# Kernel tuning notes

Hardware: AMD Instinct MI355X
Metric: run time of the kernel (lower is better)

## Reference

```python
import jax, jax.numpy as jnp
import numpy as np

N_NODES = 100000


def gcn_layer(x, edge_index, W, b):
    """PyG GCNConv: h = D^-1/2 (A+I) D^-1/2 (x W) + b, scatter-sum aggregation."""
    n = x.shape[0]
    h = x @ W  # [N, out]
    loop = jnp.arange(n, dtype=edge_index.dtype)
    src = jnp.concatenate([edge_index[0], loop])  # [E+N]
    dst = jnp.concatenate([edge_index[1], loop])
    deg = jax.ops.segment_sum(jnp.ones_like(dst, dtype=h.dtype), dst, num_segments=n)
    dinv = jnp.where(deg > 0, jax.lax.rsqrt(deg), 0.0)
    norm = dinv[src] * dinv[dst]  # [E+N]
    msg = h[src] * norm[:, None]  # gather + scale (largest intermediate)
    out = jax.ops.segment_sum(msg, dst, num_segments=n)
    return out + b


def setup_inputs() -> dict:
    key = jax.random.key(0)
    k = jax.random.split(key, 8)
    in_dim, hid_dim, out_dim = 128, 64, 112
    E = 1600000
    x = jax.random.normal(k[0], (N_NODES, in_dim), dtype=jnp.float32)
    edge_index = jax.random.randint(k[1], (2, E), 0, N_NODES, dtype=jnp.int32)
    s1 = 1.0 / np.sqrt(in_dim)
    s2 = 1.0 / np.sqrt(hid_dim)
    return {
        "x": x,
        "edge_index": edge_index,
        "W1": jax.random.uniform(k[2], (in_dim, hid_dim), jnp.float32, -s1, s1),
        "b1": jnp.zeros((hid_dim,), jnp.float32),
        "W2": jax.random.uniform(k[3], (hid_dim, hid_dim), jnp.float32, -s2, s2),
        "b2": jnp.zeros((hid_dim,), jnp.float32),
        "W3": jax.random.uniform(k[4], (hid_dim, out_dim), jnp.float32, -s2, s2),
        "b3": jnp.zeros((out_dim,), jnp.float32),
    }


def reference(x, edge_index, W1, b1, W2, b2, W3, b3):
    # eval mode: dropout is identity
    h = jax.nn.relu(gcn_layer(x, edge_index, W1, b1))
    h = jax.nn.relu(gcn_layer(h, edge_index, W2, b2))
    return gcn_layer(h, edge_index, W3, b3)
```

## Files before the change

### kernel.cpp

```cpp
#include <hip/hip_runtime.h>
#include <hip/hip_fp16.h>
#include <math.h>


#define IN_DIM 128
#define HID 64
#define OUT_DIM 112
#define LSHIFT 7
#define LMASK 127
#define MAXBUCK 1024
#define CHUNK 4096
#define CAP 4096

typedef _Float16 f16x8 __attribute__((ext_vector_type(8)));
typedef float f32x4 __attribute__((ext_vector_type(4)));

template <int K, int C, bool XH, bool DINV, bool BIAS, bool OUTH>
__device__ __forceinline__ void mfma_gemm_tile(int blk, const void* __restrict__ Xv,
                                               const float* __restrict__ W,
                                               const float* __restrict__ dinv,
                                               const float* __restrict__ bias,
                                               void* __restrict__ G, int n,
                                               _Float16* Wt) {
  constexpr int KP = K + 8;
  constexpr int NT = C / 16;
  constexpr int KS = K / 32;
  const int tid = threadIdx.x;
  for (int idx = tid; idx < K * C; idx += 256) {
    int k = idx / C, c = idx % C;
    Wt[c * KP + k] = (_Float16)W[idx];
  }
  __syncthreads();

  const int wv = tid >> 6, l = tid & 63;
  const int rbase = blk * 64 + wv * 16;
  const int kg = (l >> 4) * 8;
  const int c16 = l & 15;

  int arow = rbase + c16;
  if (arow >= n) arow = n - 1;
  f16x8 af[KS];
  if (XH) {
    const _Float16* Xh = reinterpret_cast<const _Float16*>(Xv);
#pragma unroll
    for (int ks = 0; ks < KS; ++ks)
      af[ks] = *reinterpret_cast<const f16x8*>(&Xh[(size_t)arow * K + ks * 32 + kg]);
  } else {
    const float* Xf = reinterpret_cast<const float*>(Xv);
#pragma unroll
    for (int ks = 0; ks < KS; ++ks) {
      float4 u0 = *reinterpret_cast<const float4*>(&Xf[(size_t)arow * K + ks * 32 + kg]);
      float4 u1 = *reinterpret_cast<const float4*>(&Xf[(size_t)arow * K + ks * 32 + kg + 4]);
      f16x8 a;
      a[0] = (_Float16)u0.x; a[1] = (_Float16)u0.y; a[2] = (_Float16)u0.z; a[3] = (_Float16)u0.w;
      a[4] = (_Float16)u1.x; a[5] = (_Float16)u1.y; a[6] = (_Float16)u1.z; a[7] = (_Float16)u1.w;
      af[ks] = a;
    }
  }

  f32x4 acc[NT];
#pragma unroll
  for (int nt = 0; nt < NT; ++nt) acc[nt] = (f32x4){0.f, 0.f, 0.f, 0.f};

#pragma unroll
  for (int ks = 0; ks < KS; ++ks) {
#pragma unroll
    for (int nt = 0; nt < NT; ++nt) {
      f16x8 bf = *reinterpret_cast<const f16x8*>(&Wt[(nt * 16 + c16) * KP + ks * 32 + kg]);
      acc[nt] = __builtin_amdgcn_mfma_f32_16x16x32_f16(af[ks], bf, acc[nt], 0, 0, 0);
    }
  }

#pragma unroll
  for (int r = 0; r < 4; ++r) {
    int grow = rbase + (l >> 4) * 4 + r;
    if (grow < n) {
      float s = DINV ? dinv[grow] : 1.0f;
#pragma unroll
      for (int nt = 0; nt < NT; ++nt) {
        float v = acc[nt][r] * s;
        if (BIAS) v += bias[nt * 16 + c16];
        if (OUTH)
          reinterpret_cast<__half*>(G)[(size_t)grow * C + nt * 16 + c16] = __float2half(v);
        else
          reinterpret_cast<float*>(G)[(size_t)grow * C + nt * 16 + c16] = v;
      }
    }
  }
}

template <int K, int C, bool XH, bool DINV, bool BIAS, bool OUTH>
__global__ __launch_bounds__(256) void mfma_gemm_kernel(const void* __restrict__ Xv,
                                                        const float* __restrict__ W,
                                                        const float* __restrict__ dinv,
                                                        const float* __restrict__ bias,
                                                        void* __restrict__ G, int n) {
  __shared__ _Float16 Wt[C * (K + 8)];
  mfma_gemm_tile<K, C, XH, DINV, BIAS, OUTH>(blockIdx.x, Xv, W, dinv, bias, G, n, Wt);
}

__global__ __launch_bounds__(256) void gemm1_scatter_kernel(
    const float* __restrict__ x, const float* __restrict__ W1, __half* __restrict__ gh,
    int n, const int* __restrict__ src, const int* __restrict__ dst,
    int* __restrict__ cur0, int* __restrict__ packed, int E, int nbuck, int nchunk) {
  __shared__ __align__(16) char smem[HID * (IN_DIM + 8) * 2];
  const int tid = threadIdx.x;
  if ((int)blockIdx.x < nchunk) {
    int* hist = reinterpret_cast<int*>(smem);
    int* cur = hist + MAXBUCK;
    for (int i = tid; i < nbuck; i += 256) hist[i] = 0;
    __syncthreads();
    const int lo = blockIdx.x * CHUNK;
    const int hi = min(E, lo + CHUNK);
    for (int i = lo + tid; i < hi; i += 256)
      atomicAdd(&hist[dst[i] >> LSHIFT], 1);
    __syncthreads();
    for (int b = tid; b < nbuck; b += 256) {
      int c = hist[b];
      cur[b] = (c > 0) ? atomicAdd(&cur0[b], c) : 0;
    }
    __syncthreads();
    for (int i = lo + tid; i < hi; i += 256) {
      int s = src[i], d = dst[i];
      int b = d >> LSHIFT;
      int off = atomicAdd(&cur[b], 1);
      if (off < CAP) packed[b * CAP + off] = (s << LSHIFT) | (d & LMASK);
    }
  } else {
    _Float16* Wt = reinterpret_cast<_Float16*>(smem);
    mfma_gemm_tile<IN_DIM, HID, false, false, false, true>(
        (int)blockIdx.x - nchunk, x, W1, nullptr, nullptr, gh, n, Wt);
  }
}

__global__ __launch_bounds__(256) void fine_fused_kernel(
    const int* __restrict__ packed, const int* __restrict__ cur0,
    int* __restrict__ row_start, float* __restrict__ dinv,
    int* __restrict__ ssrc, __half* __restrict__ gh, int n, int nbuck) {
  const int b = blockIdx.x;
  const int t = threadIdx.x;
  __shared__ int hist[128];
  __shared__ int pfx[128];
  __shared__ int cur[128];
  __shared__ float sdi[128];
  __shared__ int red[4];
  __shared__ int sbase;
  if (t < 128) hist[t] = 0;
  __syncthreads();
  const int cb = min(cur0[b], CAP);
  const int* pk = &packed[(size_t)b * CAP];
  for (int e = t; e < cb; e += 256) atomicAdd(&hist[pk[e] & LMASK], 1);
  int partial = 0;
  for (int i = t; i < b; i += 256) partial += min(cur0[i], CAP);
#pragma unroll
  for (int off = 1; off < 64; off <<= 1) partial += __shfl_xor(partial, off);
  const int lane = t & 63, wv = t >> 6;
  if (lane == 0) red[wv] = partial;
  __syncthreads();
  if (t == 0) sbase = red[0] + red[1] + red[2] + red[3];
  if (t < 128) pfx[t] = hist[t];
  __syncthreads();
  for (int off = 1; off < 128; off <<= 1) {
    int u = (t >= off && t < 128) ? pfx[t - off] : 0;
    __syncthreads();
    if (t < 128) pfx[t] += u;
    __syncthreads();
  }
  if (t < 128) {
    int node = b * 128 + t;
    if (node < n) {
      int rs = sbase + pfx[t] - hist[t];
      row_start[node] = rs;
      float di = 1.0f / sqrtf((float)(hist[t] + 1));
      dinv[node] = di;
      sdi[t] = di;
      cur[t] = rs;
    } else {
      sdi[t] = 0.f;
      cur[t] = 0;
    }
  }
  if (b == nbuck - 1 && t == 0) row_start[n] = sbase + cb;
  __syncthreads();
  for (int e = t; e < cb; e += 256) {
    int p = pk[e];
    int slot = atomicAdd(&cur[p & LMASK], 1);
    ssrc[slot] = p >> LSHIFT;
  }
  __half2* g2 = reinterpret_cast<__half2*>(gh);
  for (int i = t; i < 128 * 32; i += 256) {
    int nd = i >> 5;
    int node = b * 128 + nd;
    if (node < n) {
      int q = i & 31;
      float2 f = __half22float2(g2[(size_t)node * 32 + q]);
      float d = sdi[nd];
      g2[(size_t)node * 32 + q] = __floats2half2_rn(f.x * d, f.y * d);
    }
  }
}

template <int C, bool RELU, bool BIAS, bool TSCALE, bool OUTH>
__global__ __launch_bounds__(256) void agg_kernel(const __half* __restrict__ g,
                                                  const int* __restrict__ row_start,
                                                  const int* __restrict__ ssrc,
                                                  const float* __restrict__ dinv,
                                                  const float* __restrict__ bias,
                                                  void* __restrict__ out, int n) {
  static_assert(C == 64, "agg assumes 64 channels");
  const int tid = threadIdx.x;
  const int wv = tid >> 6;
  const int lane = tid & 63;
  const int h = lane >> 5;
  const int q = lane & 31;
  int node = blockIdx.x * 4 + wv;
  if (node >= n) return;
  const __half2* g2 = reinterpret_cast<const __half2*>(g);

  int e0 = row_start[node];
  int e1 = row_start[node + 1];
  int deg = e1 - e0;
  float2 acc = make_float2(0.f, 0.f);
  if (h == 0) {
    float2 sv = __half22float2(g2[(size_t)node * 32 + q]);
    acc.x = sv.x; acc.y = sv.y;
  }
  const int pairs = deg >> 1;
  const int base = e0 + h;
  int k = 0;
  for (; k + 8 <= pairs; k += 8) {
    int idx[8];
#pragma unroll
    for (int i = 0; i < 8; ++i) idx[i] = ssrc[base + 2 * (k + i)];
    __half2 v[8];
#pragma unroll
    for (int i = 0; i < 8; ++i) v[i] = g2[(size_t)idx[i] * 32 + q];
#pragma unroll
    for (int i = 0; i < 8; ++i) {
      float2 f = __half22float2(v[i]);
      acc.x += f.x; acc.y += f.y;
    }
  }
  for (; k + 2 <= pairs; k += 2) {
    int i0 = ssrc[base + 2 * k];
    int i1 = ssrc[base + 2 * (k + 1)];
    float2 f0 = __half22float2(g2[(size_t)i0 * 32 + q]);
    float2 f1 = __half22float2(g2[(size_t)i1 * 32 + q]);
    acc.x += f0.x + f1.x; acc.y += f0.y + f1.y;
  }
  for (; k < pairs; ++k) {
    int i0 = ssrc[base + 2 * k];
    float2 f = __half22float2(g2[(size_t)i0 * 32 + q]);
    acc.x += f.x; acc.y += f.y;
  }
  if ((deg & 1) && h == 0) {
    int i0 = ssrc[e1 - 1];
    float2 f = __half22float2(g2[(size_t)i0 * 32 + q]);
    acc.x += f.x; acc.y += f.y;
  }
  acc.x += __shfl_xor(acc.x, 32);
  acc.y += __shfl_xor(acc.y, 32);

  if (h == 0) {
    float di = dinv[node];
    float rx = acc.x * di, ry = acc.y * di;
    if (BIAS) {
      float2 bv = *reinterpret_cast<const float2*>(&bias[2 * q]);
      rx += bv.x; ry += bv.y;
    }
    if (RELU) { rx = fmaxf(rx, 0.f); ry = fmaxf(ry, 0.f); }
    if (TSCALE) { rx *= di; ry *= di; }
    if (OUTH) {
      reinterpret_cast<__half2*>(out)[(size_t)node * 32 + q] = __floats2half2_rn(rx, ry);
    } else {
      reinterpret_cast<float2*>(out)[(size_t)node * 32 + q] = make_float2(rx, ry);
    }
  }
}

extern "C" void kernel_launch(void* const* d_in, const int* in_sizes, int n_in,
                              void* d_out, int out_size, void* d_ws, size_t ws_size,
                              hipStream_t stream) {
  const float* x = (const float*)d_in[0];
  const int* ei = (const int*)d_in[1];
  const float* W1 = (const float*)d_in[2];
  const float* b1 = (const float*)d_in[3];
  const float* W2 = (const float*)d_in[4];
  const float* b2 = (const float*)d_in[5];
  const float* W3 = (const float*)d_in[6];
  const float* b3 = (const float*)d_in[7];
  float* out = (float*)d_out;

  const int n = in_sizes[0] / IN_DIM;
  const int E = in_sizes[1] / 2;
  const int* src = ei;
  const int* dst = ei + E;
  const int nbuck = (n + LMASK) >> LSHIFT;
  const int nchunk = (E + CHUNK - 1) / CHUNK;

  char* p = (char*)d_ws;
  auto alloc = [&](size_t bytes) {
    char* q = p;
    p += (bytes + 255) & ~(size_t)255;
    return q;
  };
  float* dinv = (float*)alloc((size_t)n * 4);
  int* row_start = (int*)alloc((size_t)(n + 1) * 4);
  int* cur0 = (int*)alloc((size_t)MAXBUCK * 4);
  int* packed = (int*)alloc((size_t)nbuck * CAP * 4);
  int* ssrc = (int*)alloc((size_t)E * 4);
  __half* gh  = (__half*)alloc((size_t)n * HID * 2);
  __half* h1h = (__half*)alloc((size_t)n * HID * 2);
  __half* th  = (__half*)alloc((size_t)n * HID * 2);
  __half* zh  = h1h;

  const int GGRID = (n + 63) / 64;

  hipMemsetAsync(cur0, 0, (size_t)MAXBUCK * 4, stream);
  gemm1_scatter_kernel<<<nchunk + GGRID, 256, 0, stream>>>(x, W1, gh, n, src, dst,
                                                           cur0, packed, E, nbuck, nchunk);
  fine_fused_kernel<<<nbuck, 256, 0, stream>>>(packed, cur0, row_start, dinv, ssrc, gh, n, nbuck);

  agg_kernel<HID, true, true, false, true><<<(n + 3) / 4, 256, 0, stream>>>(gh, row_start, ssrc, dinv, b1, h1h, n);

  mfma_gemm_kernel<HID, HID, true, true, false, true><<<GGRID, 256, 0, stream>>>(h1h, W2, dinv, nullptr, gh, n);
  agg_kernel<HID, true, true, true, true><<<(n + 3) / 4, 256, 0, stream>>>(gh, row_start, ssrc, dinv, b2, th, n);

  agg_kernel<HID, false, false, false, true><<<(n + 3) / 4, 256, 0, stream>>>(th, row_start, ssrc, dinv, nullptr, zh, n);
  mfma_gemm_kernel<HID, OUT_DIM, true, false, true, false><<<GGRID, 256, 0, stream>>>(zh, W3, nullptr, b3, out, n);
}
```

Measured before the change: 339.4 us.

## Fuse aggregation with following GEMMs and make edge bucketing deterministic

Aggregation for layers 1 and 3 is now fused with the next dense GEMM in one kernel: each block aggregates 64 nodes into global memory, syncs, then runs the MFMA tile on those rows, which removes two launches. The atomic-reservation coarse scatter is replaced by a per-chunk histogram, a per-bucket prefix kernel and a separate scatter kernel, which also drops the memset. The chunk size is doubled. The trade-off is one extra launch plus an extra pass over dst in exchange for fewer global atomics. The fused kernels also have much coarser grids, each block doing 16 aggregation iterations serially, which may reduce parallelism and latency hiding.

```diff
diff --git a/kernel.cpp b/kernel.cpp
--- a/kernel.cpp
+++ b/kernel.cpp
@@ -9,31 +9,33 @@
 #define LSHIFT 7
 #define LMASK 127
 #define MAXBUCK 1024
-#define CHUNK 4096
+#define CHUNK 8192
 #define CAP 4096
 
 typedef _Float16 f16x8 __attribute__((ext_vector_type(8)));
 typedef float f32x4 __attribute__((ext_vector_type(4)));
 
+template <int K, int C>
+__device__ __forceinline__ void stage_w(const float* __restrict__ W, _Float16* Wt) {
+  constexpr int KP = K + 8;
+  for (int idx = threadIdx.x; idx < K * C; idx += 256) {
+    int k = idx / C, c = idx % C;
+    Wt[c * KP + k] = (_Float16)W[idx];
+  }
+}
+
 template <int K, int C, bool XH, bool DINV, bool BIAS, bool OUTH>
-__device__ __forceinline__ void mfma_gemm_tile(int blk, const void* __restrict__ Xv,
-                                               const float* __restrict__ W,
-                                               const float* __restrict__ dinv,
-                                               const float* __restrict__ bias,
-                                               void* __restrict__ G, int n,
-                                               _Float16* Wt) {
+__device__ __forceinline__ void gemm_compute(int blk, const void* __restrict__ Xv,
+                                             const float* __restrict__ dinv,
+                                             const float* __restrict__ bias,
+                                             void* __restrict__ G, int n,
+                                             const _Float16* Wt) {
   constexpr int KP = K + 8;
   constexpr int NT = C / 16;
   constexpr int KS = K / 32;
   const int tid = threadIdx.x;
-  for (int idx = tid; idx < K * C; idx += 256) {
-    int k = idx / C, c = idx % C;
-    Wt[c * KP + k] = (_Float16)W[idx];
-  }
-  __syncthreads();
-
-  const int wv = tid >> 6, l = tid & 63;
-  const int rbase = blk * 64 + wv * 16;
+  const int l = tid & 63;
+  const int rbase = blk * 64 + (tid >> 6) * 16;
   const int kg = (l >> 4) * 8;
   const int c16 = l & 15;
 
@@ -89,52 +91,145 @@
   }
 }
 
-template <int K, int C, bool XH, bool DINV, bool BIAS, bool OUTH>
-__global__ __launch_bounds__(256) void mfma_gemm_kernel(const void* __restrict__ Xv,
-                                                        const float* __restrict__ W,
-                                                        const float* __restrict__ dinv,
-                                                        const float* __restrict__ bias,
-                                                        void* __restrict__ G, int n) {
-  __shared__ _Float16 Wt[C * (K + 8)];
-  mfma_gemm_tile<K, C, XH, DINV, BIAS, OUTH>(blockIdx.x, Xv, W, dinv, bias, G, n, Wt);
-}
-
-__global__ __launch_bounds__(256) void gemm1_scatter_kernel(
+template <bool RELU, bool BIAS, bool TSCALE>
+__device__ __forceinline__ void agg_item(int grp, const __half* __restrict__ g,
+                                         const int* __restrict__ row_start,
+                                         const int* __restrict__ ssrc,
+                                         const float* __restrict__ dinv,
+                                         const float* __restrict__ bias,
+                                         __half* __restrict__ out, int n) {
+  const int tid = threadIdx.x;
+  const int wv = tid >> 6;
+  const int lane = tid & 63;
+  const int h = lane >> 5;
+  const int q = lane & 31;
+  const int node = grp * 4 + wv;
+  if (node < n) {
+    const __half2* g2 = reinterpret_cast<const __half2*>(g);
+    int e0 = row_start[node];
+    int e1 = row_start[node + 1];
+    int deg = e1 - e0;
+    float2 acc = make_float2(0.f, 0.f);
+    if (h == 0) {
+      float2 sv = __half22float2(g2[(size_t)node * 32 + q]);
+      acc.x = sv.x; acc.y = sv.y;
+    }
+    const int pairs = deg >> 1;
+    const int base = e0 + h;
+    int k = 0;
+    for (; k + 8 <= pairs; k += 8) {
+      int idx[8];
+#pragma unroll
+      for (int i = 0; i < 8; ++i) idx[i] = ssrc[base + 2 * (k + i)];
+      __half2 v[8];
+#pragma unroll
+      for (int i = 0; i < 8; ++i) v[i] = g2[(size_t)idx[i] * 32 + q];
+#pragma unroll
+      for (int i = 0; i < 8; ++i) {
+        float2 f = __half22float2(v[i]);
+        acc.x += f.x; acc.y += f.y;
+      }
+    }
+    for (; k + 2 <= pairs; k += 2) {
+      int i0 = ssrc[base + 2 * k];
+      int i1 = ssrc[base + 2 * (k + 1)];
+      float2 f0 = __half22float2(g2[(size_t)i0 * 32 + q]);
+      float2 f1 = __half22float2(g2[(size_t)i1 * 32 + q]);
+      acc.x += f0.x + f1.x; acc.y += f0.y + f1.y;
+    }
+    for (; k < pairs; ++k) {
+      int i0 = ssrc[base + 2 * k];
+      float2 f = __half22float2(g2[(size_t)i0 * 32 + q]);
+      acc.x += f.x; acc.y += f.y;
+    }
+    if ((deg & 1) && h == 0) {
+      int i0 = ssrc[e1 - 1];
+      float2 f = __half22float2(g2[(size_t)i0 * 32 + q]);
+      acc.x += f.x; acc.y += f.y;
+    }
+    acc.x += __shfl_xor(acc.x, 32);
+    acc.y += __shfl_xor(acc.y, 32);
+
+    if (h == 0) {
+      float di = dinv[node];
+      float rx = acc.x * di, ry = acc.y * di;
+      if (BIAS) {
+        float2 bv = *reinterpret_cast<const float2*>(&bias[2 * q]);
+        rx += bv.x; ry += bv.y;
+      }
+      if (RELU) { rx = fmaxf(rx, 0.f); ry = fmaxf(ry, 0.f); }
+      if (TSCALE) { rx *= di; ry *= di; }
+      reinterpret_cast<__half2*>(out)[(size_t)node * 32 + q] = __floats2half2_rn(rx, ry);
+    }
+  }
+}
+
+__global__ __launch_bounds__(256) void gemm1_hist_kernel(
     const float* __restrict__ x, const float* __restrict__ W1, __half* __restrict__ gh,
-    int n, const int* __restrict__ src, const int* __restrict__ dst,
-    int* __restrict__ cur0, int* __restrict__ packed, int E, int nbuck, int nchunk) {
+    int n, const int* __restrict__ dst, int* __restrict__ H,
+    int E, int nbuck, int nchunk) {
   __shared__ __align__(16) char smem[HID * (IN_DIM + 8) * 2];
   const int tid = threadIdx.x;
   if ((int)blockIdx.x < nchunk) {
     int* hist = reinterpret_cast<int*>(smem);
-    int* cur = hist + MAXBUCK;
     for (int i = tid; i < nbuck; i += 256) hist[i] = 0;
     __syncthreads();
-    const int lo = blockIdx.x * CHUNK;
-    const int hi = min(E, lo + CHUNK);
+    int lo = blockIdx.x * CHUNK, hi = min(E, lo + CHUNK);
     for (int i = lo + tid; i < hi; i += 256)
       atomicAdd(&hist[dst[i] >> LSHIFT], 1);
     __syncthreads();
-    for (int b = tid; b < nbuck; b += 256) {
-      int c = hist[b];
-      cur[b] = (c > 0) ? atomicAdd(&cur0[b], c) : 0;
-    }
-    __syncthreads();
-    for (int i = lo + tid; i < hi; i += 256) {
-      int s = src[i], d = dst[i];
-      int b = d >> LSHIFT;
-      int off = atomicAdd(&cur[b], 1);
-      if (off < CAP) packed[b * CAP + off] = (s << LSHIFT) | (d & LMASK);
-    }
+    int* Hrow = &H[(size_t)blockIdx.x * nbuck];
+    for (int i = tid; i < nbuck; i += 256) Hrow[i] = hist[i];
   } else {
     _Float16* Wt = reinterpret_cast<_Float16*>(smem);
-    mfma_gemm_tile<IN_DIM, HID, false, false, false, true>(
-        (int)blockIdx.x - nchunk, x, W1, nullptr, nullptr, gh, n, Wt);
+    stage_w<IN_DIM, HID>(W1, Wt);
+    __syncthreads();
+    gemm_compute<IN_DIM, HID, false, false, false, true>(
+        (int)blockIdx.x - nchunk, x, nullptr, nullptr, gh, n, Wt);
+  }
+}
+
+__global__ __launch_bounds__(256) void chunk_prefix_kernel(int* __restrict__ H,
+                                                           int* __restrict__ cb,
+                                                           int nchunk, int nbuck) {
+  int wv = threadIdx.x >> 6, lane = threadIdx.x & 63;
+  int b = blockIdx.x * 4 + wv;
+  if (b >= nbuck) return;
+  int run = 0;
+  for (int c0 = 0; c0 < nchunk; c0 += 64) {
+    int c = c0 + lane;
+    int v = (c < nchunk) ? H[(size_t)c * nbuck + b] : 0;
+    int incl = v;
+#pragma unroll
+    for (int off = 1; off < 64; off <<= 1) {
+      int u = __shfl_up(incl, off);
+      if (lane >= off) incl += u;
+    }
+    if (c < nchunk) H[(size_t)c * nbuck + b] = run + incl - v;
+    run += __shfl(incl, 63);
+  }
+  if (lane == 0) cb[b] = run;
+}
+
+__global__ __launch_bounds__(256) void coarse_scatter_kernel(
+    const int* __restrict__ src, const int* __restrict__ dst,
+    const int* __restrict__ H, int* __restrict__ packed, int E, int nbuck) {
+  __shared__ int cur[MAXBUCK];
+  const int tid = threadIdx.x;
+  const int* Hrow = &H[(size_t)blockIdx.x * nbuck];
+  for (int i = tid; i < nbuck; i += 256) cur[i] = Hrow[i];
+  __syncthreads();
+  int lo = blockIdx.x * CHUNK, hi = min(E, lo + CHUNK);
+  for (int i = lo + tid; i < hi; i += 256) {
+    int s = src[i], d = dst[i];
+    int b = d >> LSHIFT;
+    int off = atomicAdd(&cur[b], 1);
+    if (off < CAP) packed[(size_t)b * CAP + off] = (s << LSHIFT) | (d & LMASK);
   }
 }
 
 __global__ __launch_bounds__(256) void fine_fused_kernel(
-    const int* __restrict__ packed, const int* __restrict__ cur0,
+    const int* __restrict__ packed, const int* __restrict__ cb,
     int* __restrict__ row_start, float* __restrict__ dinv,
     int* __restrict__ ssrc, __half* __restrict__ gh, int n, int nbuck) {
   const int b = blockIdx.x;
@@ -147,11 +242,11 @@
   __shared__ int sbase;
   if (t < 128) hist[t] = 0;
   __syncthreads();
-  const int cb = min(cur0[b], CAP);
+  const int cbb = min(cb[b], CAP);
   const int* pk = &packed[(size_t)b * CAP];
-  for (int e = t; e < cb; e += 256) atomicAdd(&hist[pk[e] & LMASK], 1);
+  for (int e = t; e < cbb; e += 256) atomicAdd(&hist[pk[e] & LMASK], 1);
   int partial = 0;
-  for (int i = t; i < b; i += 256) partial += min(cur0[i], CAP);
+  for (int i = t; i < b; i += 256) partial += min(cb[i], CAP);
 #pragma unroll
   for (int off = 1; off < 64; off <<= 1) partial += __shfl_xor(partial, off);
   const int lane = t & 63, wv = t >> 6;
@@ -180,9 +275,9 @@
       cur[t] = 0;
     }
   }
-  if (b == nbuck - 1 && t == 0) row_start[n] = sbase + cb;
-  __syncthreads();
-  for (int e = t; e < cb; e += 256) {
+  if (b == nbuck - 1 && t == 0) row_start[n] = sbase + cbb;
+  __syncthreads();
+  for (int e = t; e < cbb; e += 256) {
     int p = pk[e];
     int slot = atomicAdd(&cur[p & LMASK], 1);
     ssrc[slot] = p >> LSHIFT;
@@ -200,82 +295,44 @@
   }
 }
 
-template <int C, bool RELU, bool BIAS, bool TSCALE, bool OUTH>
+template <bool RELU, bool BIAS, bool TSCALE>
 __global__ __launch_bounds__(256) void agg_kernel(const __half* __restrict__ g,
                                                   const int* __restrict__ row_start,
                                                   const int* __restrict__ ssrc,
                                                   const float* __restrict__ dinv,
                                                   const float* __restrict__ bias,
-                                                  void* __restrict__ out, int n) {
-  static_assert(C == 64, "agg assumes 64 channels");
-  const int tid = threadIdx.x;
-  const int wv = tid >> 6;
-  const int lane = tid & 63;
-  const int h = lane >> 5;
-  const int q = lane & 31;
-  int node = blockIdx.x * 4 + wv;
-  if (node >= n) return;
-  const __half2* g2 = reinterpret_cast<const __half2*>(g);
-
-  int e0 = row_start[node];
-  int e1 = row_start[node + 1];
-  int deg = e1 - e0;
-  float2 acc = make_float2(0.f, 0.f);
-  if (h == 0) {
-    float2 sv = __half22float2(g2[(size_t)node * 32 + q]);
-    acc.x = sv.x; acc.y = sv.y;
-  }
-  const int pairs = deg >> 1;
-  const int base = e0 + h;
-  int k = 0;
-  for (; k + 8 <= pairs; k += 8) {
-    int idx[8];
-#pragma unroll
-    for (int i = 0; i < 8; ++i) idx[i] = ssrc[base + 2 * (k + i)];
-    __half2 v[8];
-#pragma unroll
-    for (int i = 0; i < 8; ++i) v[i] = g2[(size_t)idx[i] * 32 + q];
-#pragma unroll
-    for (int i = 0; i < 8; ++i) {
-      float2 f = __half22float2(v[i]);
-      acc.x += f.x; acc.y += f.y;
-    }
-  }
-  for (; k + 2 <= pairs; k += 2) {
-    int i0 = ssrc[base + 2 * k];
-    int i1 = ssrc[base + 2 * (k + 1)];
-    float2 f0 = __half22float2(g2[(size_t)i0 * 32 + q]);
-    float2 f1 = __half22float2(g2[(size_t)i1 * 32 + q]);
-    acc.x += f0.x + f1.x; acc.y += f0.y + f1.y;
-  }
-  for (; k < pairs; ++k) {
-    int i0 = ssrc[base + 2 * k];
-    float2 f = __half22float2(g2[(size_t)i0 * 32 + q]);
-    acc.x += f.x; acc.y += f.y;
-  }
-  if ((deg & 1) && h == 0) {
-    int i0 = ssrc[e1 - 1];
-    float2 f = __half22float2(g2[(size_t)i0 * 32 + q]);
-    acc.x += f.x; acc.y += f.y;
-  }
-  acc.x += __shfl_xor(acc.x, 32);
-  acc.y += __shfl_xor(acc.y, 32);
-
-  if (h == 0) {
-    float di = dinv[node];
-    float rx = acc.x * di, ry = acc.y * di;
-    if (BIAS) {
-      float2 bv = *reinterpret_cast<const float2*>(&bias[2 * q]);
-      rx += bv.x; ry += bv.y;
-    }
-    if (RELU) { rx = fmaxf(rx, 0.f); ry = fmaxf(ry, 0.f); }
-    if (TSCALE) { rx *= di; ry *= di; }
-    if (OUTH) {
-      reinterpret_cast<__half2*>(out)[(size_t)node * 32 + q] = __floats2half2_rn(rx, ry);
-    } else {
-      reinterpret_cast<float2*>(out)[(size_t)node * 32 + q] = make_float2(rx, ry);
-    }
-  }
+                                                  __half* __restrict__ out, int n) {
+  agg_item<RELU, BIAS, TSCALE>(blockIdx.x, g, row_start, ssrc, dinv, bias, out, n);
+}
+
+__global__ __launch_bounds__(256) void agg1_gemm2_kernel(
+    const __half* __restrict__ gh, const int* __restrict__ row_start,
+    const int* __restrict__ ssrc, const float* __restrict__ dinv,
+    const float* __restrict__ b1, __half* __restrict__ h1h,
+    const float* __restrict__ W2, __half* __restrict__ g2h, int n) {
+  __shared__ _Float16 Wt[HID * (HID + 8)];
+  stage_w<HID, HID>(W2, Wt);
+  const int blk = blockIdx.x;
+#pragma unroll 1
+  for (int i = 0; i < 16; ++i)
+    agg_item<true, true, false>(blk * 16 + i, gh, row_start, ssrc, dinv, b1, h1h, n);
+  __syncthreads();
+  gemm_compute<HID, HID, true, true, false, true>(blk, h1h, dinv, nullptr, g2h, n, Wt);
+}
+
+__global__ __launch_bounds__(256) void agg3_gemm3_kernel(
+    const __half* __restrict__ th, const int* __restrict__ row_start,
+    const int* __restrict__ ssrc, const float* __restrict__ dinv,
+    __half* __restrict__ h1h, const float* __restrict__ W3,
+    const float* __restrict__ b3, float* __restrict__ out, int n) {
+  __shared__ _Float16 Wt[OUT_DIM * (HID + 8)];
+  stage_w<HID, OUT_DIM>(W3, Wt);
+  const int blk = blockIdx.x;
+#pragma unroll 1
+  for (int i = 0; i < 16; ++i)
+    agg_item<false, false, false>(blk * 16 + i, th, row_start, ssrc, dinv, nullptr, h1h, n);
+  __syncthreads();
+  gemm_compute<HID, OUT_DIM, true, false, true, false>(blk, h1h, nullptr, b3, out, n, Wt);
 }
 
 extern "C" void kernel_launch(void* const* d_in, const int* in_sizes, int n_in,
@@ -306,26 +363,22 @@
   };
   float* dinv = (float*)alloc((size_t)n * 4);
   int* row_start = (int*)alloc((size_t)(n + 1) * 4);
-  int* cur0 = (int*)alloc((size_t)MAXBUCK * 4);
+  int* H = (int*)alloc((size_t)nchunk * nbuck * 4);
+  int* cb = (int*)alloc((size_t)(nbuck + 1) * 4);
   int* packed = (int*)alloc((size_t)nbuck * CAP * 4);
   int* ssrc = (int*)alloc((size_t)E * 4);
   __half* gh  = (__half*)alloc((size_t)n * HID * 2);
   __half* h1h = (__half*)alloc((size_t)n * HID * 2);
+  __half* g2h = (__half*)alloc((size_t)n * HID * 2);
   __half* th  = (__half*)alloc((size_t)n * HID * 2);
-  __half* zh  = h1h;
-
-  const int GGRID = (n + 63) / 64;
-
-  hipMemsetAsync(cur0, 0, (size_t)MAXBUCK * 4, stream);
-  gemm1_scatter_kernel<<<nchunk + GGRID, 256, 0, stream>>>(x, W1, gh, n, src, dst,
-                                                           cur0, packed, E, nbuck, nchunk);
-  fine_fused_kernel<<<nbuck, 256, 0, stream>>>(packed, cur0, row_start, dinv, ssrc, gh, n, nbuck);
-
-  agg_kernel<HID, true, true, false, true><<<(n + 3) / 4, 256, 0, stream>>>(gh, row_start, ssrc, dinv, b1, h1h, n);
-
-  mfma_gemm_kernel<HID, HID, true, true, false, true><<<GGRID, 256, 0, stream>>>(h1h, W2, dinv, nullptr, gh, n);
-  agg_kernel<HID, true, true, true, true><<<(n + 3) / 4, 256, 0, stream>>>(gh, row_start, ssrc, dinv, b2, th, n);
-
-  agg_kernel<HID, false, false, false, true><<<(n + 3) / 4, 256, 0, stream>>>(th, row_start, ssrc, dinv, nullptr, zh, n);
-  mfma_gemm_kernel<HID, OUT_DIM, true, false, true, false><<<GGRID, 256, 0, stream>>>(zh, W3, nullptr, b3, out, n);
-}
+
+  const int GG = (n + 63) / 64;
+
+  gemm1_hist_kernel<<<nchunk + GG, 256, 0, stream>>>(x, W1, gh, n, dst, H, E, nbuck, nchunk);
+  chunk_prefix_kernel<<<(nbuck + 3) / 4, 256, 0, stream>>>(H, cb, nchunk, nbuck);
+  coarse_scatter_kernel<<<nchunk, 256, 0, stream>>>(src, dst, H, packed, E, nbuck);
+  fine_fused_kernel<<<nbuck, 256, 0, stream>>>(packed, cb, row_start, dinv, ssrc, gh, n, nbuck);
+  agg1_gemm2_kernel<<<GG, 256, 0, stream>>>(gh, row_start, ssrc, dinv, b1, h1h, W2, g2h, n);
+  agg_kernel<true, true, true><<<(n + 3) / 4, 256, 0, stream>>>(g2h, row_start, ssrc, dinv, b2, th, n);
+  agg3_gemm3_kernel<<<GG, 256, 0, stream>>>(th, row_start, ssrc, dinv, h1h, W3, b3, out, n);
+}
```

Result: slower. 392.2 us (+15.6%).
